# Kernel tuning notes

Hardware: AMD Instinct MI355X
Metric: run time of the kernel (lower is better)

Reference implementation:

```python
import jax, jax.numpy as jnp
import numpy as np

BC, N, F, D = 16, 2048, 128, 128
N_EDGES = 65536
NEG_INF = -1e16
LEAK = 0.1


def setup_inputs() -> dict:
    key = jax.random.key(0)
    k_h, k_w, k_r, k_c = jax.random.split(key, 4)
    h = jax.random.normal(k_h, (BC, N, F), dtype=jnp.float32)
    # xavier_normal with gain 1.414
    w_std = 1.414 * np.sqrt(2.0 / (F + D))
    W = jax.random.normal(k_w, (F, D), dtype=jnp.float32) * w_std
    row = jax.random.randint(k_r, (N_EDGES,), 0, N, dtype=jnp.int64)
    col = jax.random.randint(k_c, (N_EDGES,), 0, N, dtype=jnp.int64)
    return {"h": h, "W": W, "row": row, "col": col}


def reference(h, W, row, col):
    bc, n, f = h.shape
    # z = h @ W : [bc, N, D]
    z = jnp.einsum("bnf,fd->bnd", h, W)
    # dense inner-product attention scores [bc, N, N]
    att = jnp.einsum("bnd,bmd->bnm", z, z)
    # leaky_relu(0.1)
    att = jnp.where(att > 0, att, LEAK * att)
    # sparse adjacency mask built from COO indices
    mask = jnp.zeros((n, n), dtype=att.dtype).at[row, col].set(1.0)
    att = att * mask[None, :, :]
    # masked_fill where value == 0 (non-edges, and incidental exact zeros)
    att = jnp.where(att == 0.0, NEG_INF, att)
    att = jax.nn.softmax(att, axis=2)
    # aggregate: [bc, N, N] @ [bc, N, D]
    return jnp.einsum("bnm,bmd->bnd", att, z)
```

## Files before the change

kernel.cpp:

```cpp
#include <hip/hip_runtime.h>

#define BC 16
#define NN 2048
#define FF 128
#define DD 128
#define NEDGES 65536
#define NEG_INF -1e16f
#define LEAK 0.1f
#define CAPR 128
#define THRS 20.0f

__global__ void __launch_bounds__(256) zedge_kernel(const float* __restrict__ h,
                                                    const float* __restrict__ W,
                                                    float* __restrict__ z,
                                                    const int* __restrict__ row,
                                                    const int* __restrict__ col,
                                                    unsigned int* __restrict__ mask) {
    const int tid = threadIdx.x;
    const int blk = blockIdx.x;

    if (blk < 256) {
        const int e = blk * 256 + tid;
        const unsigned int key = (unsigned int)row[e] * NN + (unsigned int)col[e];
        atomicOr(&mask[key >> 5], 1u << (key & 31u));
        return;
    }

    __shared__ float hs[32][FF];
    const size_t row0 = (size_t)(blk - 256) * 32;
    const float4* hv = (const float4*)(h + row0 * FF);
    float4* hsv = (float4*)&hs[0][0];
#pragma unroll
    for (int i = 0; i < 4; ++i) hsv[tid + 256 * i] = hv[tid + 256 * i];
    __syncthreads();

    const int c0 = (tid & 31) * 4;
    const int r0 = (tid >> 5) * 4;
    float acc[4][4] = {};
    for (int f = 0; f < FF; f += 4) {
        float4 a[4], bb[4];
#pragma unroll
        for (int r = 0; r < 4; ++r) a[r] = *(const float4*)&hs[r0 + r][f];
#pragma unroll
        for (int k = 0; k < 4; ++k) bb[k] = *(const float4*)&W[(f + k) * DD + c0];
#pragma unroll
        for (int r = 0; r < 4; ++r) {
            acc[r][0] += a[r].x * bb[0].x + a[r].y * bb[1].x + a[r].z * bb[2].x + a[r].w * bb[3].x;
            acc[r][1] += a[r].x * bb[0].y + a[r].y * bb[1].y + a[r].z * bb[2].y + a[r].w * bb[3].y;
            acc[r][2] += a[r].x * bb[0].z + a[r].y * bb[1].z + a[r].z * bb[2].z + a[r].w * bb[3].z;
            acc[r][3] += a[r].x * bb[0].w + a[r].y * bb[1].w + a[r].z * bb[2].w + a[r].w * bb[3].w;
        }
    }
#pragma unroll
    for (int r = 0; r < 4; ++r)
        *(float4*)&z[(row0 + r0 + r) * DD + c0] =
            make_float4(acc[r][0], acc[r][1], acc[r][2], acc[r][3]);
}

__global__ void __launch_bounds__(256) gat_kernel(const float* __restrict__ z,
                                                  const unsigned int* __restrict__ mask,
                                                  float* __restrict__ out) {
    __shared__ unsigned short hits_l[4][CAPR];
    const int tid = threadIdx.x, wv = tid >> 6, ln = tid & 63;
    const int blk = blockIdx.x;
    const int b = ((blk & 7) << 1) | (wv & 1);
    const int n = ((blk >> 3) << 1) | (wv >> 1);
    const int eq = ln >> 3, hq = ln & 7;

    unsigned int bits = mask[n * 64 + ln];
    const int cnt = __popc(bits);
    int pre = cnt;
#pragma unroll
    for (int off = 1; off <= 32; off <<= 1) {
        const int t = __shfl_up(pre, off, 64);
        if (ln >= off) pre += t;
    }
    const int total = __shfl(pre, 63, 64);
    int slot = pre - cnt;
    while (bits) {
        const int bit = __ffs(bits) - 1;
        bits &= bits - 1;
        if (slot < CAPR) hits_l[wv][slot] = (unsigned short)(ln * 32 + bit);
        ++slot;
    }
    const int nh = min(total, CAPR);
    const int hv0 = hits_l[wv][ln];
    const int hv1 = hits_l[wv][64 + ln];

    const float* zb = z + ((size_t)b << 18);
    const float4* znp = (const float4*)(zb + ((size_t)n << 7) + (hq << 4));
    const float4 a0 = znp[0], a1 = znp[1], a2 = znp[2], a3 = znp[3];

    float m = NEG_INF, l = 0.f;
    float4 acc0 = make_float4(0.f, 0.f, 0.f, 0.f), acc1 = acc0, acc2 = acc0, acc3 = acc0;

#pragma unroll 2
    for (int c0 = 0; c0 < nh; c0 += 8) {
        const int e = c0 + eq;
        const int hv = (c0 < 64) ? hv0 : hv1;
        const int he = __shfl(hv, e & 63, 64) & (NN - 1);
        const float4* zc = (const float4*)(zb + ((size_t)he << 7) + (hq << 4));
        const float4 v0 = zc[0], v1 = zc[1], v2 = zc[2], v3 = zc[3];
        float ch0 = a0.x * v0.x + a0.y * v0.y + a0.z * v0.z + a0.w * v0.w
                  + a1.x * v1.x + a1.y * v1.y + a1.z * v1.z + a1.w * v1.w;
        float ch1 = a2.x * v2.x + a2.y * v2.y + a2.z * v2.z + a2.w * v2.w
                  + a3.x * v3.x + a3.y * v3.y + a3.z * v3.z + a3.w * v3.w;
        float pt = ch0 + ch1;
        pt += __shfl_xor(pt, 1, 64);
        pt += __shfl_xor(pt, 2, 64);
        pt += __shfl_xor(pt, 4, 64);
        float sv = pt > 0.f ? pt : LEAK * pt;
        if (sv == 0.f || e >= nh) sv = NEG_INF;

        if (__any(sv - m > THRS)) {
            const float mnew = fmaxf(m, sv);
            const float alpha = __expf(m - mnew);
            m = mnew;
            l *= alpha;
            acc0.x *= alpha; acc0.y *= alpha; acc0.z *= alpha; acc0.w *= alpha;
            acc1.x *= alpha; acc1.y *= alpha; acc1.z *= alpha; acc1.w *= alpha;
            acc2.x *= alpha; acc2.y *= alpha; acc2.z *= alpha; acc2.w *= alpha;
            acc3.x *= alpha; acc3.y *= alpha; acc3.z *= alpha; acc3.w *= alpha;
        }
        const float pr = __expf(sv - m);
        l += pr;
        acc0.x += pr * v0.x; acc0.y += pr * v0.y; acc0.z += pr * v0.z; acc0.w += pr * v0.w;
        acc1.x += pr * v1.x; acc1.y += pr * v1.y; acc1.z += pr * v1.z; acc1.w += pr * v1.w;
        acc2.x += pr * v2.x; acc2.y += pr * v2.y; acc2.z += pr * v2.z; acc2.w += pr * v2.w;
        acc3.x += pr * v3.x; acc3.y += pr * v3.y; acc3.z += pr * v3.z; acc3.w += pr * v3.w;
    }

    float M = m;
#pragma unroll
    for (int off = 8; off <= 32; off <<= 1) M = fmaxf(M, __shfl_xor(M, off, 64));

    if (nh > 0 && M > 0.5f * NEG_INF) {
        const float al = __expf(m - M);
        l *= al;
        acc0.x *= al; acc0.y *= al; acc0.z *= al; acc0.w *= al;
        acc1.x *= al; acc1.y *= al; acc1.z *= al; acc1.w *= al;
        acc2.x *= al; acc2.y *= al; acc2.z *= al; acc2.w *= al;
        acc3.x *= al; acc3.y *= al; acc3.z *= al; acc3.w *= al;
#pragma unroll
        for (int off = 8; off <= 32; off <<= 1) {
            l += __shfl_xor(l, off, 64);
            acc0.x += __shfl_xor(acc0.x, off, 64); acc0.y += __shfl_xor(acc0.y, off, 64);
            acc0.z += __shfl_xor(acc0.z, off, 64); acc0.w += __shfl_xor(acc0.w, off, 64);
            acc1.x += __shfl_xor(acc1.x, off, 64); acc1.y += __shfl_xor(acc1.y, off, 64);
            acc1.z += __shfl_xor(acc1.z, off, 64); acc1.w += __shfl_xor(acc1.w, off, 64);
            acc2.x += __shfl_xor(acc2.x, off, 64); acc2.y += __shfl_xor(acc2.y, off, 64);
            acc2.z += __shfl_xor(acc2.z, off, 64); acc2.w += __shfl_xor(acc2.w, off, 64);
            acc3.x += __shfl_xor(acc3.x, off, 64); acc3.y += __shfl_xor(acc3.y, off, 64);
            acc3.z += __shfl_xor(acc3.z, off, 64); acc3.w += __shfl_xor(acc3.w, off, 64);
        }
        const float inv = 1.f / l;
        acc0.x *= inv; acc0.y *= inv; acc0.z *= inv; acc0.w *= inv;
        acc1.x *= inv; acc1.y *= inv; acc1.z *= inv; acc1.w *= inv;
        acc2.x *= inv; acc2.y *= inv; acc2.z *= inv; acc2.w *= inv;
        acc3.x *= inv; acc3.y *= inv; acc3.z *= inv; acc3.w *= inv;
    } else {
        acc0 = make_float4(0.f, 0.f, 0.f, 0.f); acc1 = acc0; acc2 = acc0; acc3 = acc0;
        for (int mm = 0; mm < NN; ++mm) {
            const float4* zr = (const float4*)(zb + ((size_t)mm << 7) + (hq << 4));
            const float4 t0 = zr[0], t1 = zr[1], t2 = zr[2], t3 = zr[3];
            acc0.x += t0.x; acc0.y += t0.y; acc0.z += t0.z; acc0.w += t0.w;
            acc1.x += t1.x; acc1.y += t1.y; acc1.z += t1.z; acc1.w += t1.w;
            acc2.x += t2.x; acc2.y += t2.y; acc2.z += t2.z; acc2.w += t2.w;
            acc3.x += t3.x; acc3.y += t3.y; acc3.z += t3.z; acc3.w += t3.w;
        }
        const float s = 1.f / NN;
        acc0.x *= s; acc0.y *= s; acc0.z *= s; acc0.w *= s;
        acc1.x *= s; acc1.y *= s; acc1.z *= s; acc1.w *= s;
        acc2.x *= s; acc2.y *= s; acc2.z *= s; acc2.w *= s;
        acc3.x *= s; acc3.y *= s; acc3.z *= s; acc3.w *= s;
    }

    if (eq < 4) {
        float4 o = acc0;
        if (eq == 1) o = acc1;
        if (eq == 2) o = acc2;
        if (eq == 3) o = acc3;
        *(float4*)(out + (((size_t)b * NN + n) << 7) + (hq << 4) + (eq << 2)) = o;
    }
}

extern "C" void kernel_launch(void* const* d_in, const int* in_sizes, int n_in,
                              void* d_out, int out_size, void* d_ws, size_t ws_size,
                              hipStream_t stream) {
    const float* h = (const float*)d_in[0];
    const float* W = (const float*)d_in[1];
    const int* row = (const int*)d_in[2];
    const int* col = (const int*)d_in[3];
    float* out = (float*)d_out;

    char* ws = (char*)d_ws;
    float* z = (float*)ws;
    unsigned int* mask = (unsigned int*)(ws + (size_t)16 * 1024 * 1024);

    hipMemsetAsync(mask, 0, (size_t)NN * NN / 8, stream);
    zedge_kernel<<<1280, 256, 0, stream>>>(h, W, z, row, col, mask);
    gat_kernel<<<(BC * NN) / 4, 256, 0, stream>>>(z, mask, out);
}
```

Measured before the change: 147.8 us.

## Build adjacency as byte mask with plain stores instead of atomic bitmask

Replaces the atomicOr bitmask construction with a byte-per-entry adjacency mask written by plain stores, and packs bytes back into 32-bit words inside the attention kernel with a multiply trick. The edge scatter and the z GEMM are split into separate kernels instead of one fused launch, and the GEMM inner loop gets unroll 2. The byte path needs 4 MB of memset and 4 MB of mask reads instead of 512 KB, and adds an extra kernel launch, in exchange for avoiding contended atomics. It falls back to the bitmask path when the workspace is too small.

```diff
diff --git a/kernel.cpp b/kernel.cpp
--- a/kernel.cpp
+++ b/kernel.cpp
@@ -10,24 +10,31 @@
 #define CAPR 128
 #define THRS 20.0f
 
-__global__ void __launch_bounds__(256) zedge_kernel(const float* __restrict__ h,
+__device__ __forceinline__ unsigned int nib4(unsigned int v) {
+    return (((v & 0x01010101u) * 0x01020408u) >> 24) & 0xFu;
+}
+
+__global__ void __launch_bounds__(256) edge_byte_kernel(const int* __restrict__ row,
+                                                        const int* __restrict__ col,
+                                                        unsigned char* __restrict__ m8) {
+    const int e = blockIdx.x * 256 + threadIdx.x;
+    m8[(size_t)row[e] * NN + (size_t)col[e]] = (unsigned char)1;
+}
+
+__global__ void __launch_bounds__(256) edge_bit_kernel(const int* __restrict__ row,
+                                                       const int* __restrict__ col,
+                                                       unsigned int* __restrict__ mask) {
+    const int e = blockIdx.x * 256 + threadIdx.x;
+    const unsigned int key = (unsigned int)row[e] * NN + (unsigned int)col[e];
+    atomicOr(&mask[key >> 5], 1u << (key & 31u));
+}
+
+__global__ void __launch_bounds__(256) zgemm_kernel(const float* __restrict__ h,
                                                     const float* __restrict__ W,
-                                                    float* __restrict__ z,
-                                                    const int* __restrict__ row,
-                                                    const int* __restrict__ col,
-                                                    unsigned int* __restrict__ mask) {
+                                                    float* __restrict__ z) {
+    __shared__ float hs[32][FF];
     const int tid = threadIdx.x;
-    const int blk = blockIdx.x;
-
-    if (blk < 256) {
-        const int e = blk * 256 + tid;
-        const unsigned int key = (unsigned int)row[e] * NN + (unsigned int)col[e];
-        atomicOr(&mask[key >> 5], 1u << (key & 31u));
-        return;
-    }
-
-    __shared__ float hs[32][FF];
-    const size_t row0 = (size_t)(blk - 256) * 32;
+    const size_t row0 = (size_t)blockIdx.x * 32;
     const float4* hv = (const float4*)(h + row0 * FF);
     float4* hsv = (float4*)&hs[0][0];
 #pragma unroll
@@ -37,6 +44,7 @@
     const int c0 = (tid & 31) * 4;
     const int r0 = (tid >> 5) * 4;
     float acc[4][4] = {};
+#pragma unroll 2
     for (int f = 0; f < FF; f += 4) {
         float4 a[4], bb[4];
 #pragma unroll
@@ -57,6 +65,7 @@
             make_float4(acc[r][0], acc[r][1], acc[r][2], acc[r][3]);
 }
 
+template <int BYTEM>
 __global__ void __launch_bounds__(256) gat_kernel(const float* __restrict__ z,
                                                   const unsigned int* __restrict__ mask,
                                                   float* __restrict__ out) {
@@ -67,7 +76,17 @@
     const int n = ((blk >> 3) << 1) | (wv >> 1);
     const int eq = ln >> 3, hq = ln & 7;
 
-    unsigned int bits = mask[n * 64 + ln];
+    unsigned int bits;
+    if constexpr (BYTEM) {
+        const unsigned int* mrow = mask + n * (NN / 4);
+        const uint4 q0 = *(const uint4*)(mrow + ln * 8);
+        const uint4 q1 = *(const uint4*)(mrow + ln * 8 + 4);
+        bits = nib4(q0.x) | (nib4(q0.y) << 4) | (nib4(q0.z) << 8) | (nib4(q0.w) << 12)
+             | (nib4(q1.x) << 16) | (nib4(q1.y) << 20) | (nib4(q1.z) << 24) | (nib4(q1.w) << 28);
+    } else {
+        bits = mask[n * 64 + ln];
+    }
+
     const int cnt = __popc(bits);
     int pre = cnt;
 #pragma unroll
@@ -195,9 +214,18 @@
 
     char* ws = (char*)d_ws;
     float* z = (float*)ws;
-    unsigned int* mask = (unsigned int*)(ws + (size_t)16 * 1024 * 1024);
-
-    hipMemsetAsync(mask, 0, (size_t)NN * NN / 8, stream);
-    zedge_kernel<<<1280, 256, 0, stream>>>(h, W, z, row, col, mask);
-    gat_kernel<<<(BC * NN) / 4, 256, 0, stream>>>(z, mask, out);
-}
+
+    if (ws_size >= (size_t)20 * 1024 * 1024 + 256) {
+        unsigned char* m8 = (unsigned char*)(ws + (size_t)16 * 1024 * 1024);
+        hipMemsetAsync(m8, 0, (size_t)NN * NN, stream);
+        edge_byte_kernel<<<NEDGES / 256, 256, 0, stream>>>(row, col, m8);
+        zgemm_kernel<<<(BC * NN) / 32, 256, 0, stream>>>(h, W, z);
+        gat_kernel<1><<<(BC * NN) / 4, 256, 0, stream>>>(z, (const unsigned int*)m8, out);
+    } else {
+        unsigned int* mask = (unsigned int*)(ws + (size_t)16 * 1024 * 1024);
+        hipMemsetAsync(mask, 0, (size_t)NN * NN / 8, stream);
+        edge_bit_kernel<<<NEDGES / 256, 256, 0, stream>>>(row, col, mask);
+        zgemm_kernel<<<(BC * NN) / 32, 256, 0, stream>>>(h, W, z);
+        gat_kernel<0><<<(BC * NN) / 4, 256, 0, stream>>>(z, mask, out);
+    }
+}
```

After: 152.5 us. 3.2% more time.

## Process two batches per wavefront in GAT and stage W in LDS

Applied to the files above, without the earlier changes.

The GAT kernel now has each wavefront handle one node across two batches, so the edge-list decode and mask bit scan are shared between batches. Each gathered neighbor index then feeds two z-row loads and two online-softmax accumulators, which halves the grid size. The z GEMM stages W through shared memory in two 64-row halves instead of reading it from global memory per thread. Edge-mask building is split out into its own kernel launch. In exchange, the GAT kernel uses many more registers, which may lower occupancy, and there is one extra kernel launch.

```diff
diff --git a/kernel.cpp b/kernel.cpp
--- a/kernel.cpp
+++ b/kernel.cpp
@@ -10,39 +10,61 @@
 #define CAPR 128
 #define THRS 20.0f
 
-__global__ void __launch_bounds__(256) zedge_kernel(const float* __restrict__ h,
+__global__ void __launch_bounds__(256) edge_kernel(const int* __restrict__ row,
+                                                   const int* __restrict__ col,
+                                                   unsigned int* __restrict__ mask) {
+    const int e = blockIdx.x * 256 + threadIdx.x;
+    const unsigned int key = (unsigned int)row[e] * NN + (unsigned int)col[e];
+    atomicOr(&mask[key >> 5], 1u << (key & 31u));
+}
+
+__global__ void __launch_bounds__(256) zgemm_kernel(const float* __restrict__ h,
                                                     const float* __restrict__ W,
-                                                    float* __restrict__ z,
-                                                    const int* __restrict__ row,
-                                                    const int* __restrict__ col,
-                                                    unsigned int* __restrict__ mask) {
+                                                    float* __restrict__ z) {
+    __shared__ float Wl[64][DD];
+    __shared__ float hs[32][FF];
     const int tid = threadIdx.x;
-    const int blk = blockIdx.x;
-
-    if (blk < 256) {
-        const int e = blk * 256 + tid;
-        const unsigned int key = (unsigned int)row[e] * NN + (unsigned int)col[e];
-        atomicOr(&mask[key >> 5], 1u << (key & 31u));
-        return;
-    }
-
-    __shared__ float hs[32][FF];
-    const size_t row0 = (size_t)(blk - 256) * 32;
+    const size_t row0 = (size_t)blockIdx.x * 32;
+
     const float4* hv = (const float4*)(h + row0 * FF);
     float4* hsv = (float4*)&hs[0][0];
 #pragma unroll
     for (int i = 0; i < 4; ++i) hsv[tid + 256 * i] = hv[tid + 256 * i];
+    const float4* wg = (const float4*)W;
+    float4* wl = (float4*)&Wl[0][0];
+#pragma unroll
+    for (int i = 0; i < 8; ++i) wl[tid + 256 * i] = wg[tid + 256 * i];
     __syncthreads();
 
     const int c0 = (tid & 31) * 4;
     const int r0 = (tid >> 5) * 4;
     float acc[4][4] = {};
-    for (int f = 0; f < FF; f += 4) {
+#pragma unroll 2
+    for (int f = 0; f < 64; f += 4) {
         float4 a[4], bb[4];
 #pragma unroll
         for (int r = 0; r < 4; ++r) a[r] = *(const float4*)&hs[r0 + r][f];
 #pragma unroll
-        for (int k = 0; k < 4; ++k) bb[k] = *(const float4*)&W[(f + k) * DD + c0];
+        for (int k = 0; k < 4; ++k) bb[k] = *(const float4*)&Wl[f + k][c0];
+#pragma unroll
+        for (int r = 0; r < 4; ++r) {
+            acc[r][0] += a[r].x * bb[0].x + a[r].y * bb[1].x + a[r].z * bb[2].x + a[r].w * bb[3].x;
+            acc[r][1] += a[r].x * bb[0].y + a[r].y * bb[1].y + a[r].z * bb[2].y + a[r].w * bb[3].y;
+            acc[r][2] += a[r].x * bb[0].z + a[r].y * bb[1].z + a[r].z * bb[2].z + a[r].w * bb[3].z;
+            acc[r][3] += a[r].x * bb[0].w + a[r].y * bb[1].w + a[r].z * bb[2].w + a[r].w * bb[3].w;
+        }
+    }
+    __syncthreads();
+#pragma unroll
+    for (int i = 0; i < 8; ++i) wl[tid + 256 * i] = wg[2048 + tid + 256 * i];
+    __syncthreads();
+#pragma unroll 2
+    for (int f = 64; f < 128; f += 4) {
+        float4 a[4], bb[4];
+#pragma unroll
+        for (int r = 0; r < 4; ++r) a[r] = *(const float4*)&hs[r0 + r][f];
+#pragma unroll
+        for (int k = 0; k < 4; ++k) bb[k] = *(const float4*)&Wl[f - 64 + k][c0];
 #pragma unroll
         for (int r = 0; r < 4; ++r) {
             acc[r][0] += a[r].x * bb[0].x + a[r].y * bb[1].x + a[r].z * bb[2].x + a[r].w * bb[3].x;
@@ -63,8 +85,8 @@
     __shared__ unsigned short hits_l[4][CAPR];
     const int tid = threadIdx.x, wv = tid >> 6, ln = tid & 63;
     const int blk = blockIdx.x;
-    const int b = ((blk & 7) << 1) | (wv & 1);
-    const int n = ((blk >> 3) << 1) | (wv >> 1);
+    const int bp = blk & 7;
+    const int n = ((blk >> 3) << 2) | wv;
     const int eq = ln >> 3, hq = ln & 7;
 
     unsigned int bits = mask[n * 64 + ln];
@@ -87,100 +109,174 @@
     const int hv0 = hits_l[wv][ln];
     const int hv1 = hits_l[wv][64 + ln];
 
-    const float* zb = z + ((size_t)b << 18);
-    const float4* znp = (const float4*)(zb + ((size_t)n << 7) + (hq << 4));
-    const float4 a0 = znp[0], a1 = znp[1], a2 = znp[2], a3 = znp[3];
-
-    float m = NEG_INF, l = 0.f;
-    float4 acc0 = make_float4(0.f, 0.f, 0.f, 0.f), acc1 = acc0, acc2 = acc0, acc3 = acc0;
+    const float* zb0 = z + ((size_t)(bp << 1) << 18);
+    const float* zb1 = zb0 + (1 << 18);
+    const float4* zn0 = (const float4*)(zb0 + ((size_t)n << 7) + (hq << 4));
+    const float4* zn1 = (const float4*)(zb1 + ((size_t)n << 7) + (hq << 4));
+    const float4 a00 = zn0[0], a01 = zn0[1], a02 = zn0[2], a03 = zn0[3];
+    const float4 a10 = zn1[0], a11 = zn1[1], a12 = zn1[2], a13 = zn1[3];
+
+    float m0 = NEG_INF, l0 = 0.f, m1 = NEG_INF, l1 = 0.f;
+    float4 c00 = make_float4(0.f, 0.f, 0.f, 0.f), c01 = c00, c02 = c00, c03 = c00;
+    float4 c10 = c00, c11 = c00, c12 = c00, c13 = c00;
 
 #pragma unroll 2
-    for (int c0 = 0; c0 < nh; c0 += 8) {
-        const int e = c0 + eq;
-        const int hv = (c0 < 64) ? hv0 : hv1;
+    for (int e0 = 0; e0 < nh; e0 += 8) {
+        const int e = e0 + eq;
+        const int hv = (e0 < 64) ? hv0 : hv1;
         const int he = __shfl(hv, e & 63, 64) & (NN - 1);
-        const float4* zc = (const float4*)(zb + ((size_t)he << 7) + (hq << 4));
-        const float4 v0 = zc[0], v1 = zc[1], v2 = zc[2], v3 = zc[3];
-        float ch0 = a0.x * v0.x + a0.y * v0.y + a0.z * v0.z + a0.w * v0.w
-                  + a1.x * v1.x + a1.y * v1.y + a1.z * v1.z + a1.w * v1.w;
-        float ch1 = a2.x * v2.x + a2.y * v2.y + a2.z * v2.z + a2.w * v2.w
-                  + a3.x * v3.x + a3.y * v3.y + a3.z * v3.z + a3.w * v3.w;
-        float pt = ch0 + ch1;
-        pt += __shfl_xor(pt, 1, 64);
-        pt += __shfl_xor(pt, 2, 64);
-        pt += __shfl_xor(pt, 4, 64);
-        float sv = pt > 0.f ? pt : LEAK * pt;
-        if (sv == 0.f || e >= nh) sv = NEG_INF;
-
-        if (__any(sv - m > THRS)) {
-            const float mnew = fmaxf(m, sv);
-            const float alpha = __expf(m - mnew);
-            m = mnew;
-            l *= alpha;
-            acc0.x *= alpha; acc0.y *= alpha; acc0.z *= alpha; acc0.w *= alpha;
-            acc1.x *= alpha; acc1.y *= alpha; acc1.z *= alpha; acc1.w *= alpha;
-            acc2.x *= alpha; acc2.y *= alpha; acc2.z *= alpha; acc2.w *= alpha;
-            acc3.x *= alpha; acc3.y *= alpha; acc3.z *= alpha; acc3.w *= alpha;
-        }
-        const float pr = __expf(sv - m);
-        l += pr;
-        acc0.x += pr * v0.x; acc0.y += pr * v0.y; acc0.z += pr * v0.z; acc0.w += pr * v0.w;
-        acc1.x += pr * v1.x; acc1.y += pr * v1.y; acc1.z += pr * v1.z; acc1.w += pr * v1.w;
-        acc2.x += pr * v2.x; acc2.y += pr * v2.y; acc2.z += pr * v2.z; acc2.w += pr * v2.w;
-        acc3.x += pr * v3.x; acc3.y += pr * v3.y; acc3.z += pr * v3.z; acc3.w += pr * v3.w;
-    }
-
-    float M = m;
-#pragma unroll
-    for (int off = 8; off <= 32; off <<= 1) M = fmaxf(M, __shfl_xor(M, off, 64));
-
-    if (nh > 0 && M > 0.5f * NEG_INF) {
-        const float al = __expf(m - M);
-        l *= al;
-        acc0.x *= al; acc0.y *= al; acc0.z *= al; acc0.w *= al;
-        acc1.x *= al; acc1.y *= al; acc1.z *= al; acc1.w *= al;
-        acc2.x *= al; acc2.y *= al; acc2.z *= al; acc2.w *= al;
-        acc3.x *= al; acc3.y *= al; acc3.z *= al; acc3.w *= al;
-#pragma unroll
-        for (int off = 8; off <= 32; off <<= 1) {
-            l += __shfl_xor(l, off, 64);
-            acc0.x += __shfl_xor(acc0.x, off, 64); acc0.y += __shfl_xor(acc0.y, off, 64);
-            acc0.z += __shfl_xor(acc0.z, off, 64); acc0.w += __shfl_xor(acc0.w, off, 64);
-            acc1.x += __shfl_xor(acc1.x, off, 64); acc1.y += __shfl_xor(acc1.y, off, 64);
-            acc1.z += __shfl_xor(acc1.z, off, 64); acc1.w += __shfl_xor(acc1.w, off, 64);
-            acc2.x += __shfl_xor(acc2.x, off, 64); acc2.y += __shfl_xor(acc2.y, off, 64);
-            acc2.z += __shfl_xor(acc2.z, off, 64); acc2.w += __shfl_xor(acc2.w, off, 64);
-            acc3.x += __shfl_xor(acc3.x, off, 64); acc3.y += __shfl_xor(acc3.y, off, 64);
-            acc3.z += __shfl_xor(acc3.z, off, 64); acc3.w += __shfl_xor(acc3.w, off, 64);
-        }
-        const float inv = 1.f / l;
-        acc0.x *= inv; acc0.y *= inv; acc0.z *= inv; acc0.w *= inv;
-        acc1.x *= inv; acc1.y *= inv; acc1.z *= inv; acc1.w *= inv;
-        acc2.x *= inv; acc2.y *= inv; acc2.z *= inv; acc2.w *= inv;
-        acc3.x *= inv; acc3.y *= inv; acc3.z *= inv; acc3.w *= inv;
+        const float4* p0 = (const float4*)(zb0 + ((size_t)he << 7) + (hq << 4));
+        const float4* p1 = (const float4*)(zb1 + ((size_t)he << 7) + (hq << 4));
+        const float4 v00 = p0[0], v01 = p0[1], v02 = p0[2], v03 = p0[3];
+        const float4 v10 = p1[0], v11 = p1[1], v12 = p1[2], v13 = p1[3];
+
+        float s00 = a00.x * v00.x + a00.y * v00.y + a00.z * v00.z + a00.w * v00.w
+                  + a01.x * v01.x + a01.y * v01.y + a01.z * v01.z + a01.w * v01.w;
+        float s01 = a02.x * v02.x + a02.y * v02.y + a02.z * v02.z + a02.w * v02.w
+                  + a03.x * v03.x + a03.y * v03.y + a03.z * v03.z + a03.w * v03.w;
+        float s10 = a10.x * v10.x + a10.y * v10.y + a10.z * v10.z + a10.w * v10.w
+                  + a11.x * v11.x + a11.y * v11.y + a11.z * v11.z + a11.w * v11.w;
+        float s11 = a12.x * v12.x + a12.y * v12.y + a12.z * v12.z + a12.w * v12.w
+                  + a13.x * v13.x + a13.y * v13.y + a13.z * v13.z + a13.w * v13.w;
+        float pt0 = s00 + s01, pt1 = s10 + s11;
+        pt0 += __shfl_xor(pt0, 1, 64);  pt1 += __shfl_xor(pt1, 1, 64);
+        pt0 += __shfl_xor(pt0, 2, 64);  pt1 += __shfl_xor(pt1, 2, 64);
+        pt0 += __shfl_xor(pt0, 4, 64);  pt1 += __shfl_xor(pt1, 4, 64);
+
+        float sv0 = pt0 > 0.f ? pt0 : LEAK * pt0;
+        float sv1 = pt1 > 0.f ? pt1 : LEAK * pt1;
+        const bool pad = e >= nh;
+        if (sv0 == 0.f || pad) sv0 = NEG_INF;
+        if (sv1 == 0.f || pad) sv1 = NEG_INF;
+
+        if (__any((sv0 - m0 > THRS) | (sv1 - m1 > THRS))) {
+            const float mn0 = fmaxf(m0, sv0), mn1 = fmaxf(m1, sv1);
+            const float al0 = __expf(m0 - mn0), al1 = __expf(m1 - mn1);
+            m0 = mn0; m1 = mn1;
+            l0 *= al0; l1 *= al1;
+            c00.x *= al0; c00.y *= al0; c00.z *= al0; c00.w *= al0;
+            c01.x *= al0; c01.y *= al0; c01.z *= al0; c01.w *= al0;
+            c02.x *= al0; c02.y *= al0; c02.z *= al0; c02.w *= al0;
+            c03.x *= al0; c03.y *= al0; c03.z *= al0; c03.w *= al0;
+            c10.x *= al1; c10.y *= al1; c10.z *= al1; c10.w *= al1;
+            c11.x *= al1; c11.y *= al1; c11.z *= al1; c11.w *= al1;
+            c12.x *= al1; c12.y *= al1; c12.z *= al1; c12.w *= al1;
+            c13.x *= al1; c13.y *= al1; c13.z *= al1; c13.w *= al1;
+        }
+        const float pr0 = __expf(sv0 - m0), pr1 = __expf(sv1 - m1);
+        l0 += pr0; l1 += pr1;
+        c00.x += pr0 * v00.x; c00.y += pr0 * v00.y; c00.z += pr0 * v00.z; c00.w += pr0 * v00.w;
+        c01.x += pr0 * v01.x; c01.y += pr0 * v01.y; c01.z += pr0 * v01.z; c01.w += pr0 * v01.w;
+        c02.x += pr0 * v02.x; c02.y += pr0 * v02.y; c02.z += pr0 * v02.z; c02.w += pr0 * v02.w;
+        c03.x += pr0 * v03.x; c03.y += pr0 * v03.y; c03.z += pr0 * v03.z; c03.w += pr0 * v03.w;
+        c10.x += pr1 * v10.x; c10.y += pr1 * v10.y; c10.z += pr1 * v10.z; c10.w += pr1 * v10.w;
+        c11.x += pr1 * v11.x; c11.y += pr1 * v11.y; c11.z += pr1 * v11.z; c11.w += pr1 * v11.w;
+        c12.x += pr1 * v12.x; c12.y += pr1 * v12.y; c12.z += pr1 * v12.z; c12.w += pr1 * v12.w;
+        c13.x += pr1 * v13.x; c13.y += pr1 * v13.y; c13.z += pr1 * v13.z; c13.w += pr1 * v13.w;
+    }
+
+    float M0 = m0, M1 = m1;
+#pragma unroll
+    for (int off = 8; off <= 32; off <<= 1) {
+        M0 = fmaxf(M0, __shfl_xor(M0, off, 64));
+        M1 = fmaxf(M1, __shfl_xor(M1, off, 64));
+    }
+    const bool ok0 = (nh > 0) && (M0 > 0.5f * NEG_INF);
+    const bool ok1 = (nh > 0) && (M1 > 0.5f * NEG_INF);
+    if (ok0) {
+        const float al = __expf(m0 - M0);
+        l0 *= al;
+        c00.x *= al; c00.y *= al; c00.z *= al; c00.w *= al;
+        c01.x *= al; c01.y *= al; c01.z *= al; c01.w *= al;
+        c02.x *= al; c02.y *= al; c02.z *= al; c02.w *= al;
+        c03.x *= al; c03.y *= al; c03.z *= al; c03.w *= al;
+    }
+    if (ok1) {
+        const float al = __expf(m1 - M1);
+        l1 *= al;
+        c10.x *= al; c10.y *= al; c10.z *= al; c10.w *= al;
+        c11.x *= al; c11.y *= al; c11.z *= al; c11.w *= al;
+        c12.x *= al; c12.y *= al; c12.z *= al; c12.w *= al;
+        c13.x *= al; c13.y *= al; c13.z *= al; c13.w *= al;
+    }
+#pragma unroll
+    for (int off = 8; off <= 32; off <<= 1) {
+        l0 += __shfl_xor(l0, off, 64); l1 += __shfl_xor(l1, off, 64);
+        c00.x += __shfl_xor(c00.x, off, 64); c00.y += __shfl_xor(c00.y, off, 64);
+        c00.z += __shfl_xor(c00.z, off, 64); c00.w += __shfl_xor(c00.w, off, 64);
+        c01.x += __shfl_xor(c01.x, off, 64); c01.y += __shfl_xor(c01.y, off, 64);
+        c01.z += __shfl_xor(c01.z, off, 64); c01.w += __shfl_xor(c01.w, off, 64);
+        c02.x += __shfl_xor(c02.x, off, 64); c02.y += __shfl_xor(c02.y, off, 64);
+        c02.z += __shfl_xor(c02.z, off, 64); c02.w += __shfl_xor(c02.w, off, 64);
+        c03.x += __shfl_xor(c03.x, off, 64); c03.y += __shfl_xor(c03.y, off, 64);
+        c03.z += __shfl_xor(c03.z, off, 64); c03.w += __shfl_xor(c03.w, off, 64);
+        c10.x += __shfl_xor(c10.x, off, 64); c10.y += __shfl_xor(c10.y, off, 64);
+        c10.z += __shfl_xor(c10.z, off, 64); c10.w += __shfl_xor(c10.w, off, 64);
+        c11.x += __shfl_xor(c11.x, off, 64); c11.y += __shfl_xor(c11.y, off, 64);
+        c11.z += __shfl_xor(c11.z, off, 64); c11.w += __shfl_xor(c11.w, off, 64);
+        c12.x += __shfl_xor(c12.x, off, 64); c12.y += __shfl_xor(c12.y, off, 64);
+        c12.z += __shfl_xor(c12.z, off, 64); c12.w += __shfl_xor(c12.w, off, 64);
+        c13.x += __shfl_xor(c13.x, off, 64); c13.y += __shfl_xor(c13.y, off, 64);
+        c13.z += __shfl_xor(c13.z, off, 64); c13.w += __shfl_xor(c13.w, off, 64);
+    }
+    if (ok0) {
+        const float inv = 1.f / l0;
+        c00.x *= inv; c00.y *= inv; c00.z *= inv; c00.w *= inv;
+        c01.x *= inv; c01.y *= inv; c01.z *= inv; c01.w *= inv;
+        c02.x *= inv; c02.y *= inv; c02.z *= inv; c02.w *= inv;
+        c03.x *= inv; c03.y *= inv; c03.z *= inv; c03.w *= inv;
     } else {
-        acc0 = make_float4(0.f, 0.f, 0.f, 0.f); acc1 = acc0; acc2 = acc0; acc3 = acc0;
+        c00 = make_float4(0.f, 0.f, 0.f, 0.f); c01 = c00; c02 = c00; c03 = c00;
         for (int mm = 0; mm < NN; ++mm) {
-            const float4* zr = (const float4*)(zb + ((size_t)mm << 7) + (hq << 4));
+            const float4* zr = (const float4*)(zb0 + ((size_t)mm << 7) + (hq << 4));
             const float4 t0 = zr[0], t1 = zr[1], t2 = zr[2], t3 = zr[3];
-            acc0.x += t0.x; acc0.y += t0.y; acc0.z += t0.z; acc0.w += t0.w;
-            acc1.x += t1.x; acc1.y += t1.y; acc1.z += t1.z; acc1.w += t1.w;
-            acc2.x += t2.x; acc2.y += t2.y; acc2.z += t2.z; acc2.w += t2.w;
-            acc3.x += t3.x; acc3.y += t3.y; acc3.z += t3.z; acc3.w += t3.w;
+            c00.x += t0.x; c00.y += t0.y; c00.z += t0.z; c00.w += t0.w;
+            c01.x += t1.x; c01.y += t1.y; c01.z += t1.z; c01.w += t1.w;
+            c02.x += t2.x; c02.y += t2.y; c02.z += t2.z; c02.w += t2.w;
+            c03.x += t3.x; c03.y += t3.y; c03.z += t3.z; c03.w += t3.w;
         }
         const float s = 1.f / NN;
-        acc0.x *= s; acc0.y *= s; acc0.z *= s; acc0.w *= s;
-        acc1.x *= s; acc1.y *= s; acc1.z *= s; acc1.w *= s;
-        acc2.x *= s; acc2.y *= s; acc2.z *= s; acc2.w *= s;
-        acc3.x *= s; acc3.y *= s; acc3.z *= s; acc3.w *= s;
-    }
-
+        c00.x *= s; c00.y *= s; c00.z *= s; c00.w *= s;
+        c01.x *= s; c01.y *= s; c01.z *= s; c01.w *= s;
+        c02.x *= s; c02.y *= s; c02.z *= s; c02.w *= s;
+        c03.x *= s; c03.y *= s; c03.z *= s; c03.w *= s;
+    }
+    if (ok1) {
+        const float inv = 1.f / l1;
+        c10.x *= inv; c10.y *= inv; c10.z *= inv; c10.w *= inv;
+        c11.x *= inv; c11.y *= inv; c11.z *= inv; c11.w *= inv;
+        c12.x *= inv; c12.y *= inv; c12.z *= inv; c12.w *= inv;
+        c13.x *= inv; c13.y *= inv; c13.z *= inv; c13.w *= inv;
+    } else {
+        c10 = make_float4(0.f, 0.f, 0.f, 0.f); c11 = c10; c12 = c10; c13 = c10;
+        for (int mm = 0; mm < NN; ++mm) {
+            const float4* zr = (const float4*)(zb1 + ((size_t)mm << 7) + (hq << 4));
+            const float4 t0 = zr[0], t1 = zr[1], t2 = zr[2], t3 = zr[3];
+            c10.x += t0.x; c10.y += t0.y; c10.z += t0.z; c10.w += t0.w;
+            c11.x += t1.x; c11.y += t1.y; c11.z += t1.z; c11.w += t1.w;
+            c12.x += t2.x; c12.y += t2.y; c12.z += t2.z; c12.w += t2.w;
+            c13.x += t3.x; c13.y += t3.y; c13.z += t3.z; c13.w += t3.w;
+        }
+        const float s = 1.f / NN;
+        c10.x *= s; c10.y *= s; c10.z *= s; c10.w *= s;
+        c11.x *= s; c11.y *= s; c11.z *= s; c11.w *= s;
+        c12.x *= s; c12.y *= s; c12.z *= s; c12.w *= s;
+        c13.x *= s; c13.y *= s; c13.z *= s; c13.w *= s;
+    }
+
+    const int b0 = bp << 1;
     if (eq < 4) {
-        float4 o = acc0;
-        if (eq == 1) o = acc1;
-        if (eq == 2) o = acc2;
-        if (eq == 3) o = acc3;
-        *(float4*)(out + (((size_t)b * NN + n) << 7) + (hq << 4) + (eq << 2)) = o;
+        float4 o = c00;
+        if (eq == 1) o = c01;
+        if (eq == 2) o = c02;
+        if (eq == 3) o = c03;
+        *(float4*)(out + (((size_t)b0 * NN + n) << 7) + (hq << 4) + (eq << 2)) = o;
+    } else {
+        float4 o = c10;
+        if (eq == 5) o = c11;
+        if (eq == 6) o = c12;
+        if (eq == 7) o = c13;
+        *(float4*)(out + (((size_t)(b0 + 1) * NN + n) << 7) + (hq << 4) + ((eq - 4) << 2)) = o;
     }
 }
 
@@ -198,6 +294,7 @@
     unsigned int* mask = (unsigned int*)(ws + (size_t)16 * 1024 * 1024);
 
     hipMemsetAsync(mask, 0, (size_t)NN * NN / 8, stream);
-    zedge_kernel<<<1280, 256, 0, stream>>>(h, W, z, row, col, mask);
-    gat_kernel<<<(BC * NN) / 4, 256, 0, stream>>>(z, mask, out);
+    edge_kernel<<<NEDGES / 256, 256, 0, stream>>>(row, col, mask);
+    zgemm_kernel<<<(BC * NN) / 32, 256, 0, stream>>>(h, W, z);
+    gat_kernel<<<(BC * NN) / 8, 256, 0, stream>>>(z, mask, out);
 }
```

After: 149.9 us. No clear change (+1.4%).

## Compute z projection with split-bf16 MFMA instead of scalar FP32 FMAs

Applied to the files above, without the earlier changes.

Replaces the scalar FP32 h@W GEMM with bf16 MFMA 16x16x32 instructions. Each operand is split into hi+lo bf16 parts and three MFMAs are issued to recover near-FP32 accuracy. W is converted to swizzled bf16 in shared memory per block, and each block now handles 64 rows, so the grid shrinks to 768 blocks. The cost is a per-block W conversion with 64KB of LDS, plus a small accuracy change from the 3-term bf16 emulation.

```diff
diff --git a/kernel.cpp b/kernel.cpp
--- a/kernel.cpp
+++ b/kernel.cpp
@@ -10,12 +10,24 @@
 #define CAPR 128
 #define THRS 20.0f
 
+typedef __attribute__((ext_vector_type(8))) short s16x8;
+typedef __attribute__((ext_vector_type(4))) float f32x4;
+
+__device__ __forceinline__ unsigned short f2bf(float x) {
+    const unsigned int u = __float_as_uint(x);
+    return (unsigned short)((u + 0x7FFFu + ((u >> 16) & 1u)) >> 16);
+}
+__device__ __forceinline__ float bf2f(unsigned short b) {
+    return __uint_as_float(((unsigned int)b) << 16);
+}
+
 __global__ void __launch_bounds__(256) zedge_kernel(const float* __restrict__ h,
                                                     const float* __restrict__ W,
                                                     float* __restrict__ z,
                                                     const int* __restrict__ row,
                                                     const int* __restrict__ col,
                                                     unsigned int* __restrict__ mask) {
+    __shared__ unsigned short Wb[FF * DD * 2];
     const int tid = threadIdx.x;
     const int blk = blockIdx.x;
 
@@ -26,35 +38,75 @@
         return;
     }
 
-    __shared__ float hs[32][FF];
-    const size_t row0 = (size_t)(blk - 256) * 32;
-    const float4* hv = (const float4*)(h + row0 * FF);
-    float4* hsv = (float4*)&hs[0][0];
-#pragma unroll
-    for (int i = 0; i < 4; ++i) hsv[tid + 256 * i] = hv[tid + 256 * i];
+    {
+        const float4* wg = (const float4*)W;
+#pragma unroll
+        for (int j = 0; j < 16; ++j) {
+            const int idx = tid + 256 * j;
+            const float4 v = wg[idx];
+            const int k = idx >> 5;
+            const int d0 = (idx & 31) << 2;
+            const int kb = k * 2;
+            const int base = kb & ~15, within = kb & 15;
+            const float vv[4] = {v.x, v.y, v.z, v.w};
+#pragma unroll
+            for (int c = 0; c < 4; ++c) {
+                const int d = d0 + c;
+                const unsigned short hi = f2bf(vv[c]);
+                const unsigned short lo = f2bf(vv[c] - bf2f(hi));
+                const int off = d * 512 + ((base ^ ((d & 7) << 4)) | within);
+                Wb[off >> 1] = hi;
+                Wb[(off + 256) >> 1] = lo;
+            }
+        }
+    }
     __syncthreads();
 
-    const int c0 = (tid & 31) * 4;
-    const int r0 = (tid >> 5) * 4;
-    float acc[4][4] = {};
-    for (int f = 0; f < FF; f += 4) {
-        float4 a[4], bb[4];
-#pragma unroll
-        for (int r = 0; r < 4; ++r) a[r] = *(const float4*)&hs[r0 + r][f];
-#pragma unroll
-        for (int k = 0; k < 4; ++k) bb[k] = *(const float4*)&W[(f + k) * DD + c0];
-#pragma unroll
-        for (int r = 0; r < 4; ++r) {
-            acc[r][0] += a[r].x * bb[0].x + a[r].y * bb[1].x + a[r].z * bb[2].x + a[r].w * bb[3].x;
-            acc[r][1] += a[r].x * bb[0].y + a[r].y * bb[1].y + a[r].z * bb[2].y + a[r].w * bb[3].y;
-            acc[r][2] += a[r].x * bb[0].z + a[r].y * bb[1].z + a[r].z * bb[2].z + a[r].w * bb[3].z;
-            acc[r][3] += a[r].x * bb[0].w + a[r].y * bb[1].w + a[r].z * bb[2].w + a[r].w * bb[3].w;
-        }
-    }
-#pragma unroll
-    for (int r = 0; r < 4; ++r)
-        *(float4*)&z[(row0 + r0 + r) * DD + c0] =
-            make_float4(acc[r][0], acc[r][1], acc[r][2], acc[r][3]);
+    const int ln = tid & 63, wv = tid >> 6;
+    const int m0 = (blk - 256) * 64 + wv * 16;
+    const int mr = m0 + (ln & 15);
+    const int koct = (ln >> 4) * 8;
+
+    s16x8 ah[4], al[4];
+#pragma unroll
+    for (int k0 = 0; k0 < 4; ++k0) {
+        const float* hp = h + (size_t)mr * FF + k0 * 32 + koct;
+        const float4 p = *(const float4*)hp;
+        const float4 q = *(const float4*)(hp + 4);
+        const float x[8] = {p.x, p.y, p.z, p.w, q.x, q.y, q.z, q.w};
+        s16x8 hi8, lo8;
+#pragma unroll
+        for (int i = 0; i < 8; ++i) {
+            const unsigned short hb = f2bf(x[i]);
+            hi8[i] = (short)hb;
+            lo8[i] = (short)f2bf(x[i] - bf2f(hb));
+        }
+        ah[k0] = hi8; al[k0] = lo8;
+    }
+
+    f32x4 acc[8] = {};
+#pragma unroll
+    for (int k0 = 0; k0 < 4; ++k0) {
+#pragma unroll
+        for (int dt = 0; dt < 8; ++dt) {
+            const int d = dt * 16 + (ln & 15);
+            const int kb = (k0 * 32 + koct) * 2;
+            const int off = d * 512 + (kb ^ ((d & 7) << 4));
+            const s16x8 bh = *(const s16x8*)((const char*)Wb + off);
+            const s16x8 bl = *(const s16x8*)((const char*)Wb + off + 256);
+            acc[dt] = __builtin_amdgcn_mfma_f32_16x16x32_bf16(ah[k0], bh, acc[dt], 0, 0, 0);
+            acc[dt] = __builtin_amdgcn_mfma_f32_16x16x32_bf16(al[k0], bh, acc[dt], 0, 0, 0);
+            acc[dt] = __builtin_amdgcn_mfma_f32_16x16x32_bf16(ah[k0], bl, acc[dt], 0, 0, 0);
+        }
+    }
+
+    const int dcol = ln & 15;
+    const int rbase = m0 + (ln >> 4) * 4;
+#pragma unroll
+    for (int dt = 0; dt < 8; ++dt)
+#pragma unroll
+        for (int r = 0; r < 4; ++r)
+            z[(size_t)(rbase + r) * DD + dt * 16 + dcol] = acc[dt][r];
 }
 
 __global__ void __launch_bounds__(256) gat_kernel(const float* __restrict__ z,
@@ -198,6 +250,6 @@
     unsigned int* mask = (unsigned int*)(ws + (size_t)16 * 1024 * 1024);
 
     hipMemsetAsync(mask, 0, (size_t)NN * NN / 8, stream);
-    zedge_kernel<<<1280, 256, 0, stream>>>(h, W, z, row, col, mask);
+    zedge_kernel<<<768, 256, 0, stream>>>(h, W, z, row, col, mask);
     gat_kernel<<<(BC * NN) / 4, 256, 0, stream>>>(z, mask, out);
 }
```

Result: faster. 144.6 us (-2.2%).
